# Performance work log

Measured on AMD Instinct MI355X. Metric: run time of the kernel, lower is better.

## Reference

```python
import jax, jax.numpy as jnp
import numpy as np

N = 50000
E = 800000
IN = 128
H = 128
OUT = 64
L = 2
THETA = 1.0
SCALE = 2.0


def setup_inputs() -> dict:
    key = jax.random.key(0)
    ks = jax.random.split(key, 12)
    g = lambda k, s: (jax.random.normal(k, s, jnp.float32) * 0.05)
    return {
        "x": jax.random.normal(ks[0], (N, IN), jnp.float32),
        "edge_index": jax.random.randint(ks[1], (2, E), 0, N),
        "mlp_w1": g(ks[2], (IN, 512)), "mlp_b1": jnp.zeros((512,), jnp.float32),
        "mlp_w2": g(ks[3], (512, 64)), "mlp_b2": jnp.zeros((64,), jnp.float32),
        "mlp_w3": g(ks[4], (64, OUT)), "mlp_b3": jnp.zeros((OUT,), jnp.float32),
        "parsing": jnp.ones((L, OUT, OUT), jnp.float32) / SCALE,
        "lin0_w": g(ks[5], (IN, H)), "lin0_b": jnp.zeros((H,), jnp.float32),
        "lin1_w": g(ks[6], (H, OUT)), "lin1_b": jnp.zeros((OUT,), jnp.float32),
        "conv_w1": g(ks[7], (L, H, H)),
        "conv_w2": g(ks[8], (L, H, H)),
    }


def reference(x, edge_index, mlp_w1, mlp_b1, mlp_w2, mlp_b2, mlp_w3, mlp_b3,
              parsing, lin0_w, lin0_b, lin1_w, lin1_b, conv_w1, conv_w2):
    row, col = edge_index[0], edge_index[1]  # start, end

    # --- learn_soft_edge3 (algebraically exact reduction of outer-product + bmm + diag) ---
    h = jax.nn.relu(x @ mlp_w1 + mlp_b1)
    h = jax.nn.relu(h @ mlp_w2 + mlp_b2)
    logits = h @ mlp_w3 + mlp_b3                      # [N, OUT]
    P = jax.nn.relu(SCALE * parsing[0])               # [OUT, OUT]
    # diag(outer(start,end) @ P)[e,c] = start[e,c] * (end @ P)[e,c]
    ew = jnp.sum(logits[row] * (logits @ P)[col], axis=1)  # [E]
    mean = ew.mean()
    var = jnp.var(ew, ddof=1)                          # torch.var is unbiased
    ew = (ew - mean) * jnp.sqrt(jnp.float32(1e-4) / var) + 1.0

    # --- GCN2 stack ---
    x0 = jax.nn.relu(x @ lin0_w + lin0_b)              # [N, H]
    # gcn_norm with self loops (weight 1)
    loop = jnp.arange(N)
    r = jnp.concatenate([row, loop])
    c = jnp.concatenate([col, loop])
    w = jnp.concatenate([ew, jnp.ones((N,), ew.dtype)])
    deg = jax.ops.segment_sum(w, c, num_segments=N)
    dinv = jnp.where(deg > 0, jax.lax.rsqrt(jnp.where(deg > 0, deg, 1.0)), 0.0)
    norm = dinv[r] * w * dinv[c]                       # [E+N]

    hcur = x0
    alpha = 0.0
    for ln in range(L):
        agg = jax.ops.segment_sum(norm[:, None] * hcur[r], c, num_segments=N)  # [N, H]
        agg = agg * (1.0 - alpha)
        x0a = alpha * x0
        beta = float(np.log(THETA / (ln + 1) + 1.0))
        out = (1.0 - beta) * agg + beta * (agg @ conv_w1[ln]) \
            + (1.0 - beta) * x0a + beta * (x0a @ conv_w2[ln])
        hcur = jax.nn.relu(out)
    return hcur @ lin1_w + lin1_b                      # [N, OUT]
```

## Files before the change

### kernel.cpp

```cpp
#include <hip/hip_runtime.h>
#include <hip/hip_bf16.h>
#include <hip/hip_fp16.h>
#include <math.h>

#define NN 50000
#define NE 800000

typedef __attribute__((ext_vector_type(8))) short bf16x8;
typedef __attribute__((ext_vector_type(4))) float f32x4;

__device__ __forceinline__ short f2bf(float f){
  unsigned u = __float_as_uint(f);
  unsigned r = (u + 0x7fffu + ((u >> 16) & 1u)) >> 16;
  return (short)r;
}
__device__ __forceinline__ float bf2f(short s){
  return __uint_as_float(((unsigned)(unsigned short)s) << 16);
}

__device__ __forceinline__ unsigned f2fp8(float f){
  __half h = __float2half(f * 0.00390625f);
  unsigned hb = (unsigned)__half_as_ushort(h);
  unsigned s = hb >> 15;
  unsigned mag = hb & 0x7fffu;
  mag = mag + 0x3fu + ((mag >> 7) & 1u);
  unsigned m8 = mag >> 7;
  if (m8 > 0x7eu) m8 = 0x7eu;
  return (s << 7) | m8;
}
__device__ __forceinline__ void fp8x4_dec(unsigned u, float2& lo, float2& hi){
  unsigned l = ((u & 0x80u) << 8) | ((u & 0x7fu) << 7)
             | ((u & 0x8000u) << 16) | ((u & 0x7f00u) << 15);
  unsigned h = ((u & 0x800000u) >> 8) | ((u & 0x7f0000u) >> 9)
             | (u & 0x80000000u) | ((u & 0x7f000000u) >> 1);
  __half2 hl = *(__half2*)&l;
  __half2 hh = *(__half2*)&h;
  lo = __half22float2(hl);
  hi = __half22float2(hh);
}
__device__ __forceinline__ float fp8_dot4(unsigned a, unsigned b){
  float2 al, ah, bl, bh;
  fp8x4_dec(a, al, ah); fp8x4_dec(b, bl, bh);
  return al.x*bl.x + al.y*bl.y + ah.x*bh.x + ah.y*bh.y;
}

__global__ __launch_bounds__(256) void zero_cnt_k(int* __restrict__ cnt, float* __restrict__ scal, int n){
  int i = blockIdx.x*256 + threadIdx.x;
  if (i < n) cnt[i] = 0;
  if (blockIdx.x == 0 && threadIdx.x < 16) scal[threadIdx.x] = 0.0f;
}

__global__ __launch_bounds__(256) void prep_k(const float* __restrict__ w1,
    const float* __restrict__ w2, const float* __restrict__ w3, const float* __restrict__ pars,
    const float* __restrict__ lin0w, const float* __restrict__ cw1, const float* __restrict__ lin1w,
    short* __restrict__ w1t, short* __restrict__ w2t, short* __restrict__ w3t, short* __restrict__ Pt,
    short* __restrict__ lin0wt, short* __restrict__ cw1t0, short* __restrict__ cw1t1,
    short* __restrict__ lin1wt){
  int idx = blockIdx.x*256 + threadIdx.x;
  if (idx < 65536){
    int n = idx >> 7, k = idx & 127;
    w1t[idx] = f2bf(w1[k*512 + n]);
  } else if (idx < 98304){
    int i = idx - 65536; int n = i >> 9, k = i & 511;
    w2t[i] = f2bf(w2[k*64 + n]);
  } else if (idx < 102400){
    int i = idx - 98304; int n = i >> 6, k = i & 63;
    w3t[i] = f2bf(w3[k*64 + n]);
  } else if (idx < 106496){
    int i = idx - 102400; int n = i >> 6, k = i & 63;
    Pt[i] = f2bf(fmaxf(2.f*pars[k*64 + n], 0.f));
  } else if (idx < 122880){
    int i = idx - 106496; int n = i >> 7, k = i & 127;
    lin0wt[i] = f2bf(lin0w[k*128 + n]);
  } else if (idx < 139264){
    int i = idx - 122880; int n = i >> 7, k = i & 127;
    cw1t0[i] = f2bf(cw1[k*128 + n]);
  } else if (idx < 155648){
    int i = idx - 139264; int n = i >> 7, k = i & 127;
    cw1t1[i] = f2bf(cw1[16384 + k*128 + n]);
  } else if (idx < 163840){
    int i = idx - 155648; int n = i >> 7, k = i & 127;
    lin1wt[i] = f2bf(lin1w[k*64 + n]);
  }
}

__global__ __launch_bounds__(256) void mlp_mfma_k(
    const float* __restrict__ x,
    const short* __restrict__ w1t, const float* __restrict__ b1,
    const short* __restrict__ w2t, const float* __restrict__ b2,
    const short* __restrict__ w3t, const float* __restrict__ b3,
    const short* __restrict__ Pt,
    unsigned char* __restrict__ lg8, unsigned char* __restrict__ lgp8,
    short* __restrict__ xb, int M)
{
  __shared__ short xs [32][136];
  __shared__ short h1s[32][264];
  __shared__ short h2s[32][72];
  __shared__ short lgs[32][72];
  const int t = threadIdx.x;
  const int wave = t >> 6, lane = t & 63;
  const int quad = lane >> 4, l16 = lane & 15;
  const int m0 = blockIdx.x * 32;

  for (int task = t; task < 512; task += 256){
    int row = task >> 4, c0 = (task & 15) * 8;
    float4 v0 = make_float4(0,0,0,0), v1 = v0;
    int gm = m0 + row;
    if (gm < M){
      v0 = *(const float4*)(x + (size_t)gm*128 + c0);
      v1 = *(const float4*)(x + (size_t)gm*128 + c0 + 4);
    }
    bf16x8 s;
    s[0]=f2bf(v0.x); s[1]=f2bf(v0.y); s[2]=f2bf(v0.z); s[3]=f2bf(v0.w);
    s[4]=f2bf(v1.x); s[5]=f2bf(v1.y); s[6]=f2bf(v1.z); s[7]=f2bf(v1.w);
    *(bf16x8*)&xs[row][c0] = s;
    if (gm < M) *(bf16x8*)(xb + (size_t)gm*128 + c0) = s;
  }
  __syncthreads();

  f32x4 acc2[2];
  acc2[0] = (f32x4){0.f,0.f,0.f,0.f}; acc2[1] = acc2[0];
  const int n2 = wave*16 + l16;

  #pragma unroll
  for (int half = 0; half < 2; half++){
    {
      f32x4 acc[2][4];
      #pragma unroll
      for (int mt=0;mt<2;mt++)
        #pragma unroll
        for (int nt=0;nt<4;nt++) acc[mt][nt] = (f32x4){0.f,0.f,0.f,0.f};
      #pragma unroll
      for (int k0 = 0; k0 < 128; k0 += 32){
        bf16x8 a0 = *(const bf16x8*)&xs[l16     ][k0 + quad*8];
        bf16x8 a1 = *(const bf16x8*)&xs[16 + l16][k0 + quad*8];
        #pragma unroll
        for (int nt = 0; nt < 4; nt++){
          int n = half*256 + wave*64 + nt*16 + l16;
          bf16x8 b = *(const bf16x8*)(w1t + (size_t)n*128 + k0 + quad*8);
          acc[0][nt] = __builtin_amdgcn_mfma_f32_16x16x32_bf16(a0, b, acc[0][nt], 0,0,0);
          acc[1][nt] = __builtin_amdgcn_mfma_f32_16x16x32_bf16(a1, b, acc[1][nt], 0,0,0);
        }
      }
      #pragma unroll
      for (int nt = 0; nt < 4; nt++){
        int n  = half*256 + wave*64 + nt*16 + l16;
        int cl = wave*64 + nt*16 + l16;
        float bb = b1[n];
        #pragma unroll
        for (int mt = 0; mt < 2; mt++){
          #pragma unroll
          for (int r = 0; r < 4; r++){
            int row = mt*16 + quad*4 + r;
            h1s[row][cl] = f2bf(fmaxf(acc[mt][nt][r] + bb, 0.f));
          }
        }
      }
    }
    __syncthreads();

    for (int k0 = 0; k0 < 256; k0 += 32){
      bf16x8 b  = *(const bf16x8*)(w2t + (size_t)n2*512 + half*256 + k0 + quad*8);
      bf16x8 a0 = *(const bf16x8*)&h1s[l16     ][k0 + quad*8];
      bf16x8 a1 = *(const bf16x8*)&h1s[16 + l16][k0 + quad*8];
      acc2[0] = __builtin_amdgcn_mfma_f32_16x16x32_bf16(a0, b, acc2[0], 0,0,0);
      acc2[1] = __builtin_amdgcn_mfma_f32_16x16x32_bf16(a1, b, acc2[1], 0,0,0);
    }
    if (half == 0) __syncthreads();
  }

  {
    float bb = b2[n2];
    #pragma unroll
    for (int mt = 0; mt < 2; mt++)
      #pragma unroll
      for (int r = 0; r < 4; r++)
        h2s[mt*16 + quad*4 + r][n2] = f2bf(fmaxf(acc2[mt][r] + bb, 0.f));
  }
  __syncthreads();

  {
    f32x4 acc[2];
    acc[0] = (f32x4){0.f,0.f,0.f,0.f}; acc[1] = acc[0];
    for (int k0 = 0; k0 < 64; k0 += 32){
      bf16x8 b  = *(const bf16x8*)(w3t + (size_t)n2*64 + k0 + quad*8);
      bf16x8 a0 = *(const bf16x8*)&h2s[l16     ][k0 + quad*8];
      bf16x8 a1 = *(const bf16x8*)&h2s[16 + l16][k0 + quad*8];
      acc[0] = __builtin_amdgcn_mfma_f32_16x16x32_bf16(a0, b, acc[0], 0,0,0);
      acc[1] = __builtin_amdgcn_mfma_f32_16x16x32_bf16(a1, b, acc[1], 0,0,0);
    }
    float bb = b3[n2];
    #pragma unroll
    for (int mt = 0; mt < 2; mt++)
      #pragma unroll
      for (int r = 0; r < 4; r++)
        lgs[mt*16 + quad*4 + r][n2] = f2bf(acc[mt][r] + bb);
  }
  __syncthreads();

  {
    f32x4 acc[2];
    acc[0] = (f32x4){0.f,0.f,0.f,0.f}; acc[1] = acc[0];
    for (int k0 = 0; k0 < 64; k0 += 32){
      bf16x8 b  = *(const bf16x8*)(Pt + (size_t)n2*64 + k0 + quad*8);
      bf16x8 a0 = *(const bf16x8*)&lgs[l16     ][k0 + quad*8];
      bf16x8 a1 = *(const bf16x8*)&lgs[16 + l16][k0 + quad*8];
      acc[0] = __builtin_amdgcn_mfma_f32_16x16x32_bf16(a0, b, acc[0], 0,0,0);
      acc[1] = __builtin_amdgcn_mfma_f32_16x16x32_bf16(a1, b, acc[1], 0,0,0);
    }
    #pragma unroll
    for (int mt = 0; mt < 2; mt++)
      #pragma unroll
      for (int r = 0; r < 4; r++)
        h2s[mt*16 + quad*4 + r][n2] = f2bf(acc[mt][r]);
  }
  __syncthreads();

  {
    int row = t >> 3, c0 = (t & 7) * 8;
    int gm = m0 + row;
    if (gm < M){
      const short* pl = &lgs[row][c0];
      const short* pp = &h2s[row][c0];
      unsigned a0 = 0, a1 = 0, b0 = 0, b1 = 0;
      #pragma unroll
      for (int j = 0; j < 4; j++){
        a0 |= f2fp8(bf2f(pl[j]))     << (8*j);
        a1 |= f2fp8(bf2f(pl[4+j]))   << (8*j);
        b0 |= f2fp8(bf2f(pp[j]))     << (8*j);
        b1 |= f2fp8(bf2f(pp[4+j]))   << (8*j);
      }
      uint2 av; av.x = a0; av.y = a1;
      uint2 bv; bv.x = b0; bv.y = b1;
      *(uint2*)(lg8  + (size_t)gm*64 + c0) = av;
      *(uint2*)(lgp8 + (size_t)gm*64 + c0) = bv;
    }
  }
}

template<int NT, bool RELU, bool RESID, bool BF16OUT>
__global__ __launch_bounds__(256) void bgemm_k(
    const short* __restrict__ A, const short* __restrict__ Bt,
    const float* __restrict__ bias, const short* __restrict__ extra,
    float* __restrict__ C, short* __restrict__ Cb, int M, float beta)
{
  const int N = NT*64;
  __shared__ short As[32][136];
  const int t = threadIdx.x;
  const int wave = t >> 6, lane = t & 63;
  const int quad = lane >> 4, l16 = lane & 15;
  const int m0 = blockIdx.x * 32;

  for (int task = t; task < 512; task += 256){
    int row = task >> 4, c0 = (task & 15) * 8;
    bf16x8 v = {0,0,0,0,0,0,0,0};
    if (m0 + row < M) v = *(const bf16x8*)(A + (size_t)(m0+row)*128 + c0);
    *(bf16x8*)&As[row][c0] = v;
  }
  __syncthreads();

  f32x4 acc[2][NT];
  #pragma unroll
  for (int mt=0;mt<2;mt++)
    #pragma unroll
    for (int nt=0;nt<NT;nt++) acc[mt][nt] = (f32x4){0.f,0.f,0.f,0.f};

  #pragma unroll
  for (int k0 = 0; k0 < 128; k0 += 32){
    bf16x8 a0 = *(const bf16x8*)&As[l16     ][k0 + quad*8];
    bf16x8 a1 = *(const bf16x8*)&As[16 + l16][k0 + quad*8];
    #pragma unroll
    for (int nt = 0; nt < NT; nt++){
      int n = (wave*NT + nt)*16 + l16;
      bf16x8 b = *(const bf16x8*)(Bt + (size_t)n*128 + k0 + quad*8);
      acc[0][nt] = __builtin_amdgcn_mfma_f32_16x16x32_bf16(a0, b, acc[0][nt], 0,0,0);
      acc[1][nt] = __builtin_amdgcn_mfma_f32_16x16x32_bf16(a1, b, acc[1][nt], 0,0,0);
    }
  }

  #pragma unroll
  for (int nt = 0; nt < NT; nt++){
    int n = (wave*NT + nt)*16 + l16;
    float bb = (bias != nullptr) ? bias[n] : 0.f;
    #pragma unroll
    for (int mt = 0; mt < 2; mt++){
      #pragma unroll
      for (int r = 0; r < 4; r++){
        int gm = m0 + mt*16 + quad*4 + r;
        if (gm >= M) continue;
        float v = acc[mt][nt][r];
        if (RESID){
          float ex = bf2f(extra[(size_t)gm*N + n]);
          v = beta*v + (1.f - beta)*ex;
        }
        v += bb;
        if (RELU) v = fmaxf(v, 0.f);
        if (BF16OUT) Cb[(size_t)gm*N + n] = f2bf(v);
        else         C [(size_t)gm*N + n] = v;
      }
    }
  }
}

__global__ __launch_bounds__(256) void count_k(const int* __restrict__ col, int* __restrict__ cnt,
    int* __restrict__ rank, int E){
  int i = (blockIdx.x*256 + threadIdx.x)*4;
  if (i + 3 < E){
    int4 c = *(const int4*)(col + i);
    int r0 = atomicAdd(&cnt[c.x], 1);
    int r1 = atomicAdd(&cnt[c.y], 1);
    int r2 = atomicAdd(&cnt[c.z], 1);
    int r3 = atomicAdd(&cnt[c.w], 1);
    *(int4*)(rank + i) = make_int4(r0, r1, r2, r3);
  } else {
    for (; i < E; i++) rank[i] = atomicAdd(&cnt[col[i]], 1);
  }
}

__global__ __launch_bounds__(256) void scan_sums_k(const int* __restrict__ cnt, int* __restrict__ bsum, int n){
  __shared__ int s[256];
  const int t = threadIdx.x;
  int i = blockIdx.x*1024 + t*4;
  int4 v = make_int4(0,0,0,0);
  if (i + 3 < n) v = *(const int4*)(cnt + i);
  else {
    if (i   < n) v.x = cnt[i];
    if (i+1 < n) v.y = cnt[i+1];
    if (i+2 < n) v.z = cnt[i+2];
    if (i+3 < n) v.w = cnt[i+3];
  }
  s[t] = v.x + v.y + v.z + v.w;
  __syncthreads();
  for (int st = 128; st; st >>= 1){
    if (t < st) s[t] += s[t + st];
    __syncthreads();
  }
  if (t == 0) bsum[blockIdx.x] = s[0];
}

__global__ __launch_bounds__(64) void scan_bsum_k(int* __restrict__ bsum, int nb){
  int t = threadIdx.x;
  int own = (t < nb) ? bsum[t] : 0;
  int v = own;
  #pragma unroll
  for (int off = 1; off < 64; off <<= 1){
    int o = __shfl_up(v, off, 64);
    if (t >= off) v += o;
  }
  if (t < nb) bsum[t] = v - own;
}

__global__ __launch_bounds__(256) void scan_final_k(const int* __restrict__ cnt, const int* __restrict__ bsum,
    int* __restrict__ off, int n, int total){
  __shared__ int s[256];
  const int t = threadIdx.x;
  int i = blockIdx.x*1024 + t*4;
  int4 v = make_int4(0,0,0,0);
  if (i + 3 < n) v = *(const int4*)(cnt + i);
  else {
    if (i   < n) v.x = cnt[i];
    if (i+1 < n) v.y = cnt[i+1];
    if (i+2 < n) v.z = cnt[i+2];
    if (i+3 < n) v.w = cnt[i+3];
  }
  int tsum = v.x + v.y + v.z + v.w;
  s[t] = tsum;
  __syncthreads();
  #pragma unroll
  for (int st = 1; st < 256; st <<= 1){
    int a = (t >= st) ? s[t - st] : 0;
    __syncthreads();
    s[t] += a;
    __syncthreads();
  }
  int base = s[t] - tsum + bsum[blockIdx.x];
  int o0 = base, o1 = o0 + v.x, o2 = o1 + v.y, o3 = o2 + v.z;
  if (i   < n) off[i]   = o0;
  if (i+1 < n) off[i+1] = o1;
  if (i+2 < n) off[i+2] = o2;
  if (i+3 < n) off[i+3] = o3;
  if (blockIdx.x == 0 && t == 0) off[n] = total;
}

__global__ __launch_bounds__(256) void scatter_k(const int* __restrict__ row, const int* __restrict__ col,
    const int* __restrict__ off, const int* __restrict__ rank,
    int2* __restrict__ csr_sd, int E){
  int i = (blockIdx.x*256 + threadIdx.x)*4;
  if (i + 3 < E){
    int4 r = *(const int4*)(row + i);
    int4 c = *(const int4*)(col + i);
    int4 k = *(const int4*)(rank + i);
    int o0 = off[c.x], o1 = off[c.y], o2 = off[c.z], o3 = off[c.w];
    int2 p0; p0.x = r.x; p0.y = c.x;
    int2 p1; p1.x = r.y; p1.y = c.y;
    int2 p2; p2.x = r.z; p2.y = c.z;
    int2 p3; p3.x = r.w; p3.y = c.w;
    csr_sd[o0 + k.x] = p0;
    csr_sd[o1 + k.y] = p1;
    csr_sd[o2 + k.z] = p2;
    csr_sd[o3 + k.w] = p3;
  } else {
    for (; i < E; i++){
      int2 p; p.x = row[i]; p.y = col[i];
      csr_sd[off[col[i]] + rank[i]] = p;
    }
  }
}

__global__ __launch_bounds__(256) void ew2_k(const unsigned char* __restrict__ lg8,
    const unsigned char* __restrict__ lgp8,
    const int2* __restrict__ sd,
    float* __restrict__ w, float* __restrict__ scal, int E){
  const int t = threadIdx.x;
  const int lane = t & 63, wid = t >> 6;
  const int g = lane >> 4, q = lane & 15;
  const int gid = (blockIdx.x*4 + wid)*4 + g;
  const int ngroups = gridDim.x*16;
  float s = 0.f, ss = 0.f;
  for (int base = gid*4; base < E; base += ngroups*4){
    int4 p01 = *(const int4*)(sd + base);
    int4 p23 = *(const int4*)(sd + base + 2);
    unsigned a0 = *(const unsigned*)(lg8  + (size_t)p01.x*64 + q*4);
    unsigned a1 = *(const unsigned*)(lg8  + (size_t)p01.z*64 + q*4);
    unsigned a2 = *(const unsigned*)(lg8  + (size_t)p23.x*64 + q*4);
    unsigned a3 = *(const unsigned*)(lg8  + (size_t)p23.z*64 + q*4);
    unsigned b0 = *(const unsigned*)(lgp8 + (size_t)p01.y*64 + q*4);
    unsigned b1 = *(const unsigned*)(lgp8 + (size_t)p01.w*64 + q*4);
    unsigned b2 = *(const unsigned*)(lgp8 + (size_t)p23.y*64 + q*4);
    unsigned b3 = *(const unsigned*)(lgp8 + (size_t)p23.w*64 + q*4);
    float v0 = fp8_dot4(a0, b0);
    float v1 = fp8_dot4(a1, b1);
    float v2 = fp8_dot4(a2, b2);
    float v3 = fp8_dot4(a3, b3);
    #pragma unroll
    for (int o = 1; o < 16; o <<= 1){
      v0 += __shfl_xor(v0, o); v1 += __shfl_xor(v1, o);
      v2 += __shfl_xor(v2, o); v3 += __shfl_xor(v3, o);
    }
    if (q == 0){
      float4 vv = make_float4(v0*65536.f, v1*65536.f, v2*65536.f, v3*65536.f);
      *(float4*)(w + base) = vv;
      s  += vv.x + vv.y + vv.z + vv.w;
      ss += vv.x*vv.x + vv.y*vv.y + vv.z*vv.z + vv.w*vv.w;
    }
  }
  #pragma unroll
  for (int o = 1; o < 64; o <<= 1){ s += __shfl_xor(s, o); ss += __shfl_xor(ss, o); }
  __shared__ float ls[4], lss[4];
  if (lane == 0){ ls[wid] = s; lss[wid] = ss; }
  __syncthreads();
  if (t == 0){
    atomicAdd(&scal[0], ls[0]+ls[1]+ls[2]+ls[3]);
    atomicAdd(&scal[1], lss[0]+lss[1]+lss[2]+lss[3]);
  }
}

__global__ void finalize_k(float* scal, int E){
  double sum = (double)scal[0], sumsq = (double)scal[1];
  double mean = sum / (double)E;
  double var  = (sumsq - sum*sum/(double)E) / (double)(E-1);
  scal[2] = (float)mean;
  scal[3] = (float)sqrt(1e-4 / var);
}

__global__ __launch_bounds__(256) void degnorm_k(float* __restrict__ w, const int* __restrict__ off,
    const float* __restrict__ scal, float* __restrict__ dinv, int Nn){
  int n = blockIdx.x*256 + threadIdx.x;
  if (n < Nn){
    float mean = scal[2], k = scal[3];
    int s = off[n], e = off[n+1];
    float d = 1.0f;
    for (int j = s; j < e; j++){
      float v = (w[j] - mean) * k + 1.0f;
      w[j] = v;
      d += v;
    }
    dinv[n] = (d > 0.f) ? rsqrtf(d) : 0.f;
  }
}

__global__ __launch_bounds__(256) void wfin_k(float* __restrict__ w, const int2* __restrict__ sd,
    const float* __restrict__ dinv, int E){
  int i = (blockIdx.x*256 + threadIdx.x)*4;
  if (i + 3 < E){
    int4 p01 = *(const int4*)(sd + i);
    int4 p23 = *(const int4*)(sd + i + 2);
    float4 wv = *(const float4*)(w + i);
    float d0 = dinv[p01.x]*dinv[p01.y];
    float d1 = dinv[p01.z]*dinv[p01.w];
    float d2 = dinv[p23.x]*dinv[p23.y];
    float d3 = dinv[p23.z]*dinv[p23.w];
    wv.x *= d0; wv.y *= d1; wv.z *= d2; wv.w *= d3;
    *(float4*)(w + i) = wv;
  } else {
    for (; i < E; i++){
      int2 p = sd[i];
      w[i] = w[i] * dinv[p.y] * dinv[p.x];
    }
  }
}

__global__ __launch_bounds__(256) void agg_gather_k(const short* __restrict__ hb,
    const int* __restrict__ off, const int2* __restrict__ sd, const float* __restrict__ w,
    const float* __restrict__ dinv, short* __restrict__ aggb, int Nn){
  int n = blockIdx.x*4 + (threadIdx.x >> 6);
  int lane = threadIdx.x & 63;
  if (n >= Nn) return;
  float d = dinv[n];
  short2 hv = *(const short2*)(hb + (size_t)n*128 + lane*2);
  float acc0 = d*d*bf2f(hv.x), acc1 = d*d*bf2f(hv.y);
  int s = off[n], e = off[n+1];
  int j = s;
  for (; j + 7 < e; j += 8){
    int4 p0 = *(const int4*)(sd + j);
    int4 p1 = *(const int4*)(sd + j + 2);
    int4 p2 = *(const int4*)(sd + j + 4);
    int4 p3 = *(const int4*)(sd + j + 6);
    float4 w0 = *(const float4*)(w + j);
    float4 w1 = *(const float4*)(w + j + 4);
    short2 h0 = *(const short2*)(hb + (size_t)p0.x*128 + lane*2);
    short2 h1 = *(const short2*)(hb + (size_t)p0.z*128 + lane*2);
    short2 h2 = *(const short2*)(hb + (size_t)p1.x*128 + lane*2);
    short2 h3 = *(const short2*)(hb + (size_t)p1.z*128 + lane*2);
    short2 h4 = *(const short2*)(hb + (size_t)p2.x*128 + lane*2);
    short2 h5 = *(const short2*)(hb + (size_t)p2.z*128 + lane*2);
    short2 h6 = *(const short2*)(hb + (size_t)p3.x*128 + lane*2);
    short2 h7 = *(const short2*)(hb + (size_t)p3.z*128 + lane*2);
    acc0 += w0.x*bf2f(h0.x) + w0.y*bf2f(h1.x) + w0.z*bf2f(h2.x) + w0.w*bf2f(h3.x)
          + w1.x*bf2f(h4.x) + w1.y*bf2f(h5.x) + w1.z*bf2f(h6.x) + w1.w*bf2f(h7.x);
    acc1 += w0.x*bf2f(h0.y) + w0.y*bf2f(h1.y) + w0.z*bf2f(h2.y) + w0.w*bf2f(h3.y)
          + w1.x*bf2f(h4.y) + w1.y*bf2f(h5.y) + w1.z*bf2f(h6.y) + w1.w*bf2f(h7.y);
  }
  for (; j < e; j++){
    int2 p = sd[j];
    short2 h0 = *(const short2*)(hb + (size_t)p.x*128 + lane*2);
    float w0 = w[j];
    acc0 += w0*bf2f(h0.x); acc1 += w0*bf2f(h0.y);
  }
  short2 o; o.x = f2bf(acc0); o.y = f2bf(acc1);
  *(short2*)(aggb + (size_t)n*128 + lane*2) = o;
}

extern "C" void kernel_launch(void* const* d_in, const int* in_sizes, int n_in,
                              void* d_out, int out_size, void* d_ws, size_t ws_size,
                              hipStream_t stream){
  const float* x      = (const float*)d_in[0];
  const int*   ei     = (const int*)  d_in[1];
  const float* w1     = (const float*)d_in[2];
  const float* b1     = (const float*)d_in[3];
  const float* w2     = (const float*)d_in[4];
  const float* b2     = (const float*)d_in[5];
  const float* w3     = (const float*)d_in[6];
  const float* b3     = (const float*)d_in[7];
  const float* pars   = (const float*)d_in[8];
  const float* lin0w  = (const float*)d_in[9];
  const float* lin0b  = (const float*)d_in[10];
  const float* lin1w  = (const float*)d_in[11];
  const float* lin1b  = (const float*)d_in[12];
  const float* cw1    = (const float*)d_in[13];
  float* out          = (float*)d_out;

  float* ws = (float*)d_ws;
  int*   cnt     = (int*)(ws + 0);
  int*   off     = (int*)(ws + 50048);
  int2*  csr_sd  = (int2*)(ws + 150144);
  int*   bsum    = (int*)(ws + 1750400);
  short* lin0wt  = (short*)(ws + 1751000);
  short* cw1t0   = lin0wt + 16384;
  short* cw1t1   = cw1t0 + 16384;
  short* lin1wt  = cw1t1 + 16384;
  unsigned char* lg8  = (unsigned char*)(ws + 1800000);
  unsigned char* lgp8 = (unsigned char*)(ws + 2600000);
  float* csr_w2  = ws + 3400000;
  float* dinv    = ws + 5800000;
  float* scal    = ws + 5850048;
  short* bufAb   = (short*)(ws + 5900000);
  short* bufCb   = (short*)(ws + 9100000);
  short* aggb    = (short*)(ws + 12300000);
  short* bufBb   = (short*)(ws + 15500000);
  short* w1t     = (short*)(ws + 18700000);
  short* w2t     = w1t + 65536;
  short* w3t     = w2t + 32768;
  short* Pt      = w3t + 4096;
  short* xb      = (short*)(ws + 18800000);
  int*   rank    = (int*)(ws + 22000000);

  const int Mn = NN, E = NE;
  const int* erow = ei;
  const int* ecol = ei + E;
  const float beta0 = 0.69314718055994530942f;
  const float beta1 = 0.40546510810816438198f;
  const int nScanB = (Mn + 1023) / 1024;
  const int nGB = (Mn + 31) / 32;
  const int nE4 = (E/4 + 255) / 256;

  zero_cnt_k<<<(Mn+255)/256, 256, 0, stream>>>(cnt, scal, Mn);
  prep_k<<<(163840+255)/256, 256, 0, stream>>>(w1, w2, w3, pars, lin0w, cw1, lin1w,
                                               w1t, w2t, w3t, Pt, lin0wt, cw1t0, cw1t1, lin1wt);
  count_k<<<nE4, 256, 0, stream>>>(ecol, cnt, rank, E);
  scan_sums_k<<<nScanB, 256, 0, stream>>>(cnt, bsum, Mn);
  scan_bsum_k<<<1, 64, 0, stream>>>(bsum, nScanB);
  scan_final_k<<<nScanB, 256, 0, stream>>>(cnt, bsum, off, Mn, E);
  scatter_k<<<nE4, 256, 0, stream>>>(erow, ecol, off, rank, csr_sd, E);
  mlp_mfma_k<<<(Mn+31)/32, 256, 0, stream>>>(x, w1t, b1, w2t, b2, w3t, b3, Pt,
                                             lg8, lgp8, xb, Mn);
  ew2_k<<<1024, 256, 0, stream>>>(lg8, lgp8, csr_sd, csr_w2, scal, E);
  finalize_k<<<1, 1, 0, stream>>>(scal, E);
  degnorm_k<<<(Mn+255)/256, 256, 0, stream>>>(csr_w2, off, scal, dinv, Mn);
  wfin_k<<<nE4, 256, 0, stream>>>(csr_w2, csr_sd, dinv, E);
  bgemm_k<2,true,false,true><<<nGB, 256, 0, stream>>>(xb, lin0wt, lin0b, nullptr, nullptr, bufAb, Mn, 0.f);
  agg_gather_k<<<(Mn+3)/4, 256, 0, stream>>>(bufAb, off, csr_sd, csr_w2, dinv, aggb, Mn);
  bgemm_k<2,true,true,true><<<nGB, 256, 0, stream>>>(aggb, cw1t0, nullptr, aggb, nullptr, bufCb, Mn, beta0);
  agg_gather_k<<<(Mn+3)/4, 256, 0, stream>>>(bufCb, off, csr_sd, csr_w2, dinv, aggb, Mn);
  bgemm_k<2,true,true,true><<<nGB, 256, 0, stream>>>(aggb, cw1t1, nullptr, aggb, nullptr, bufBb, Mn, beta1);
  bgemm_k<1,false,false,false><<<nGB, 256, 0, stream>>>(bufBb, lin1wt, lin1b, nullptr, out, nullptr, Mn, 0.f);
}
```

Before: 395.9 us.

## Fold symmetric GCN normalization into GEMM epilogues and drop small kernels

Removes the per-edge weight finalization pass by factoring dinv[src]*dinv[dst] out of edge weights: source rows are prescaled by dinv in the preceding GEMM epilogue, and the gather multiplies the sum by dinv of the destination. Also merges counter zeroing into prep_k, folds the block-sum scan into scan_final_k, and computes mean/variance inside degnorm_k, eliminating four launches. The cost is a full edge-array pass traded for an extra per-row multiply plus redundant per-thread double math. It also changes where bf16 rounding happens, so numerics shift slightly.

```diff
diff --git a/kernel.cpp b/kernel.cpp
--- a/kernel.cpp
+++ b/kernel.cpp
@@ -44,19 +44,15 @@
   return al.x*bl.x + al.y*bl.y + ah.x*bh.x + ah.y*bh.y;
 }
 
-__global__ __launch_bounds__(256) void zero_cnt_k(int* __restrict__ cnt, float* __restrict__ scal, int n){
-  int i = blockIdx.x*256 + threadIdx.x;
-  if (i < n) cnt[i] = 0;
-  if (blockIdx.x == 0 && threadIdx.x < 16) scal[threadIdx.x] = 0.0f;
-}
-
 __global__ __launch_bounds__(256) void prep_k(const float* __restrict__ w1,
     const float* __restrict__ w2, const float* __restrict__ w3, const float* __restrict__ pars,
     const float* __restrict__ lin0w, const float* __restrict__ cw1, const float* __restrict__ lin1w,
     short* __restrict__ w1t, short* __restrict__ w2t, short* __restrict__ w3t, short* __restrict__ Pt,
     short* __restrict__ lin0wt, short* __restrict__ cw1t0, short* __restrict__ cw1t1,
-    short* __restrict__ lin1wt){
+    short* __restrict__ lin1wt, int* __restrict__ cnt, float* __restrict__ scal){
   int idx = blockIdx.x*256 + threadIdx.x;
+  if (idx < NN) cnt[idx] = 0;
+  if (idx < 16) scal[idx] = 0.0f;
   if (idx < 65536){
     int n = idx >> 7, k = idx & 127;
     w1t[idx] = f2bf(w1[k*512 + n]);
@@ -238,10 +234,11 @@
   }
 }
 
-template<int NT, bool RELU, bool RESID, bool BF16OUT>
+template<int NT, bool RELU, bool RESID, bool BF16OUT, bool SCALEROW>
 __global__ __launch_bounds__(256) void bgemm_k(
     const short* __restrict__ A, const short* __restrict__ Bt,
     const float* __restrict__ bias, const short* __restrict__ extra,
+    const float* __restrict__ dinvp,
     float* __restrict__ C, short* __restrict__ Cb, int M, float beta)
 {
   const int N = NT*64;
@@ -295,6 +292,7 @@
         }
         v += bb;
         if (RELU) v = fmaxf(v, 0.f);
+        if (SCALEROW) v *= dinvp[gm];
         if (BF16OUT) Cb[(size_t)gm*N + n] = f2bf(v);
         else         C [(size_t)gm*N + n] = v;
       }
@@ -338,22 +336,17 @@
   if (t == 0) bsum[blockIdx.x] = s[0];
 }
 
-__global__ __launch_bounds__(64) void scan_bsum_k(int* __restrict__ bsum, int nb){
-  int t = threadIdx.x;
-  int own = (t < nb) ? bsum[t] : 0;
-  int v = own;
-  #pragma unroll
-  for (int off = 1; off < 64; off <<= 1){
-    int o = __shfl_up(v, off, 64);
-    if (t >= off) v += o;
-  }
-  if (t < nb) bsum[t] = v - own;
-}
-
 __global__ __launch_bounds__(256) void scan_final_k(const int* __restrict__ cnt, const int* __restrict__ bsum,
-    int* __restrict__ off, int n, int total){
+    int* __restrict__ off, int n, int total, int nb){
   __shared__ int s[256];
+  __shared__ int basebs;
   const int t = threadIdx.x;
+  if (t < 64){
+    int v = (t < nb && t < (int)blockIdx.x) ? bsum[t] : 0;
+    #pragma unroll
+    for (int o = 1; o < 64; o <<= 1) v += __shfl_xor(v, o);
+    if (t == 0) basebs = v;
+  }
   int i = blockIdx.x*1024 + t*4;
   int4 v = make_int4(0,0,0,0);
   if (i + 3 < n) v = *(const int4*)(cnt + i);
@@ -373,7 +366,7 @@
     s[t] += a;
     __syncthreads();
   }
-  int base = s[t] - tsum + bsum[blockIdx.x];
+  int base = s[t] - tsum + basebs;
   int o0 = base, o1 = o0 + v.x, o2 = o1 + v.y, o3 = o2 + v.z;
   if (i   < n) off[i]   = o0;
   if (i+1 < n) off[i+1] = o1;
@@ -455,19 +448,15 @@
   }
 }
 
-__global__ void finalize_k(float* scal, int E){
-  double sum = (double)scal[0], sumsq = (double)scal[1];
-  double mean = sum / (double)E;
-  double var  = (sumsq - sum*sum/(double)E) / (double)(E-1);
-  scal[2] = (float)mean;
-  scal[3] = (float)sqrt(1e-4 / var);
-}
-
 __global__ __launch_bounds__(256) void degnorm_k(float* __restrict__ w, const int* __restrict__ off,
-    const float* __restrict__ scal, float* __restrict__ dinv, int Nn){
+    const float* __restrict__ scal, float* __restrict__ dinv, int Nn, int E){
   int n = blockIdx.x*256 + threadIdx.x;
   if (n < Nn){
-    float mean = scal[2], k = scal[3];
+    double sum = (double)scal[0], sumsq = (double)scal[1];
+    double mean_d = sum / (double)E;
+    double var    = (sumsq - sum*sum/(double)E) / (double)(E-1);
+    float mean = (float)mean_d;
+    float k    = (float)sqrt(1e-4 / var);
     int s = off[n], e = off[n+1];
     float d = 1.0f;
     for (int j = s; j < e; j++){
@@ -476,27 +465,6 @@
       d += v;
     }
     dinv[n] = (d > 0.f) ? rsqrtf(d) : 0.f;
-  }
-}
-
-__global__ __launch_bounds__(256) void wfin_k(float* __restrict__ w, const int2* __restrict__ sd,
-    const float* __restrict__ dinv, int E){
-  int i = (blockIdx.x*256 + threadIdx.x)*4;
-  if (i + 3 < E){
-    int4 p01 = *(const int4*)(sd + i);
-    int4 p23 = *(const int4*)(sd + i + 2);
-    float4 wv = *(const float4*)(w + i);
-    float d0 = dinv[p01.x]*dinv[p01.y];
-    float d1 = dinv[p01.z]*dinv[p01.w];
-    float d2 = dinv[p23.x]*dinv[p23.y];
-    float d3 = dinv[p23.z]*dinv[p23.w];
-    wv.x *= d0; wv.y *= d1; wv.z *= d2; wv.w *= d3;
-    *(float4*)(w + i) = wv;
-  } else {
-    for (; i < E; i++){
-      int2 p = sd[i];
-      w[i] = w[i] * dinv[p.y] * dinv[p.x];
-    }
   }
 }
 
@@ -508,7 +476,7 @@
   if (n >= Nn) return;
   float d = dinv[n];
   short2 hv = *(const short2*)(hb + (size_t)n*128 + lane*2);
-  float acc0 = d*d*bf2f(hv.x), acc1 = d*d*bf2f(hv.y);
+  float acc0 = bf2f(hv.x), acc1 = bf2f(hv.y);
   int s = off[n], e = off[n+1];
   int j = s;
   for (; j + 7 < e; j += 8){
@@ -537,6 +505,7 @@
     float w0 = w[j];
     acc0 += w0*bf2f(h0.x); acc1 += w0*bf2f(h0.y);
   }
+  acc0 *= d; acc1 *= d;
   short2 o; o.x = f2bf(acc0); o.y = f2bf(acc1);
   *(short2*)(aggb + (size_t)n*128 + lane*2) = o;
 }
@@ -594,24 +563,21 @@
   const int nGB = (Mn + 31) / 32;
   const int nE4 = (E/4 + 255) / 256;
 
-  zero_cnt_k<<<(Mn+255)/256, 256, 0, stream>>>(cnt, scal, Mn);
   prep_k<<<(163840+255)/256, 256, 0, stream>>>(w1, w2, w3, pars, lin0w, cw1, lin1w,
-                                               w1t, w2t, w3t, Pt, lin0wt, cw1t0, cw1t1, lin1wt);
+                                               w1t, w2t, w3t, Pt, lin0wt, cw1t0, cw1t1, lin1wt,
+                                               cnt, scal);
   count_k<<<nE4, 256, 0, stream>>>(ecol, cnt, rank, E);
   scan_sums_k<<<nScanB, 256, 0, stream>>>(cnt, bsum, Mn);
-  scan_bsum_k<<<1, 64, 0, stream>>>(bsum, nScanB);
-  scan_final_k<<<nScanB, 256, 0, stream>>>(cnt, bsum, off, Mn, E);
+  scan_final_k<<<nScanB, 256, 0, stream>>>(cnt, bsum, off, Mn, E, nScanB);
   scatter_k<<<nE4, 256, 0, stream>>>(erow, ecol, off, rank, csr_sd, E);
   mlp_mfma_k<<<(Mn+31)/32, 256, 0, stream>>>(x, w1t, b1, w2t, b2, w3t, b3, Pt,
                                              lg8, lgp8, xb, Mn);
   ew2_k<<<1024, 256, 0, stream>>>(lg8, lgp8, csr_sd, csr_w2, scal, E);
-  finalize_k<<<1, 1, 0, stream>>>(scal, E);
-  degnorm_k<<<(Mn+255)/256, 256, 0, stream>>>(csr_w2, off, scal, dinv, Mn);
-  wfin_k<<<nE4, 256, 0, stream>>>(csr_w2, csr_sd, dinv, E);
-  bgemm_k<2,true,false,true><<<nGB, 256, 0, stream>>>(xb, lin0wt, lin0b, nullptr, nullptr, bufAb, Mn, 0.f);
+  degnorm_k<<<(Mn+255)/256, 256, 0, stream>>>(csr_w2, off, scal, dinv, Mn, E);
+  bgemm_k<2,true,false,true,true><<<nGB, 256, 0, stream>>>(xb, lin0wt, lin0b, nullptr, dinv, nullptr, bufAb, Mn, 0.f);
   agg_gather_k<<<(Mn+3)/4, 256, 0, stream>>>(bufAb, off, csr_sd, csr_w2, dinv, aggb, Mn);
-  bgemm_k<2,true,true,true><<<nGB, 256, 0, stream>>>(aggb, cw1t0, nullptr, aggb, nullptr, bufCb, Mn, beta0);
+  bgemm_k<2,true,true,true,true><<<nGB, 256, 0, stream>>>(aggb, cw1t0, nullptr, aggb, dinv, nullptr, bufCb, Mn, beta0);
   agg_gather_k<<<(Mn+3)/4, 256, 0, stream>>>(bufCb, off, csr_sd, csr_w2, dinv, aggb, Mn);
-  bgemm_k<2,true,true,true><<<nGB, 256, 0, stream>>>(aggb, cw1t1, nullptr, aggb, nullptr, bufBb, Mn, beta1);
-  bgemm_k<1,false,false,false><<<nGB, 256, 0, stream>>>(bufBb, lin1wt, lin1b, nullptr, out, nullptr, Mn, 0.f);
-}
+  bgemm_k<2,true,true,true,false><<<nGB, 256, 0, stream>>>(aggb, cw1t1, nullptr, aggb, nullptr, nullptr, bufBb, Mn, beta1);
+  bgemm_k<1,false,false,false,false><<<nGB, 256, 0, stream>>>(bufBb, lin1wt, lin1b, nullptr, nullptr, out, nullptr, Mn, 0.f);
+}
```

New measurement: 383.2 us. 3.2% less time.
